# Kernel tuning notes

Measured on AMD Instinct MI355X. Metric: run time of the kernel, lower is better.

Reference implementation:

```python
import jax, jax.numpy as jnp
import numpy as np

SEGMENT_LENGTHS = [1024, 4096]
DILATION_RATES = [1, 2]
HILBERT_CHUNK = 4096
B, N, H, D = 2, 4096, 16, 64


def _hilbert_mapping(n: int) -> np.ndarray:
    """Replicates _generate_hilbert_curve: gather indices for a length-n chunk."""
    if n <= 64:
        return np.arange(n, dtype=np.int64)
    size = 1
    while size * size < n:
        size *= 2

    def d2xy(nn, d):
        x = y = 0
        s = 1
        while s < nn:
            rx = 1 if (d // 2) & 1 else 0
            ry = 1 if (d ^ rx) & 1 else 0
            if ry == 0:
                if rx == 1:
                    x, y = nn - 1 - x, nn - 1 - y
                x, y = y, x
            x += s * rx
            y += s * ry
            d //= 4
            s *= 2
        return x, y

    mapping = np.zeros(n, dtype=np.int64)
    h2l = {}
    for i in range(min(n, size * size)):
        x, y = d2xy(size, i)
        li = y * size + x
        if li < n:
            h2l[i] = li
    hidx = 0
    for i in sorted(h2l):
        mapping[h2l[i]] = hidx
        hidx += 1
    return mapping


def _apply_hilbert(t: jnp.ndarray) -> jnp.ndarray:
    # t: [b, n, h, d]; reorder sequence within HILBERT_CHUNK-sized chunks.
    n = t.shape[1]
    chunks = []
    for start in range(0, n, HILBERT_CHUNK):
        end = min(start + HILBERT_CHUNK, n)
        m = jnp.asarray(_hilbert_mapping(end - start))
        chunks.append(t[:, start:end][:, m])
    return jnp.concatenate(chunks, axis=1) if len(chunks) > 1 else chunks[0]


def _dilation_indices(s: int, r: int, offset: int) -> np.ndarray:
    # Replicates _create_dilation_pattern
    idx = np.arange(offset, s, r, dtype=np.int64)
    expected = (s + r - 1 - offset) // r
    if idx.shape[0] > expected:
        idx = idx[:expected]
    elif idx.shape[0] < expected:
        pad = np.arange(expected - idx.shape[0], dtype=np.int64) % idx.shape[0]
        idx = np.concatenate([idx, idx[pad]])
    return idx


def _dilated_attention(q, k, v):
    # LongNet-style dilated attention: heads partitioned across groups;
    # each group attends within segments over dilated positions.
    b, n, h, d = q.shape
    G = len(SEGMENT_LENGTHS)
    hg = h // G
    scale = 1.0 / np.sqrt(d).astype(np.float32)
    out = jnp.zeros_like(q)
    for g, (s, r) in enumerate(zip(SEGMENT_LENGTHS, DILATION_RATES)):
        offset = g % r
        idx = jnp.asarray(_dilation_indices(s, r, offset))
        hs = slice(g * hg, (g + 1) * hg)
        # [b, n//s, s, hg, d] -> dilated [b, n//s, s/r, hg, d]
        qg = q[:, :, hs].reshape(b, n // s, s, hg, d)[:, :, idx]
        kg = k[:, :, hs].reshape(b, n // s, s, hg, d)[:, :, idx]
        vg = v[:, :, hs].reshape(b, n // s, s, hg, d)[:, :, idx]
        att = jnp.einsum('bgqhd,bgkhd->bghqk', qg, kg) * scale
        att = jax.nn.softmax(att, axis=-1)
        og = jnp.einsum('bghqk,bgkhd->bgqhd', att, vg)
        full = jnp.zeros((b, n // s, s, hg, d), q.dtype).at[:, :, idx].set(og)
        out = out.at[:, :, hs].set(full.reshape(b, n, hg, d))
    return out


def setup_inputs() -> dict:
    key = jax.random.key(0)
    kq, kk, kv = jax.random.split(key, 3)
    q = jax.random.normal(kq, (B, N, H, D), dtype=jnp.float32)
    k = jax.random.normal(kk, (B, N, H, D), dtype=jnp.float32)
    v = jax.random.normal(kv, (B, N, H, D), dtype=jnp.float32)
    return {'q': q, 'k': k, 'v': v}


def reference(q, k, v):
    k_h = _apply_hilbert(k)
    v_h = _apply_hilbert(v)
    return _dilated_attention(q, k_h, v_h)
```

## Files before the change

kernel.cpp:

```cpp
#include <hip/hip_runtime.h>
#include <hip/hip_bf16.h>

#define N_ 4096
#define H_ 16
#define D_ 64
#define G1ROWOFF 65536

typedef __attribute__((ext_vector_type(4))) float f32x4;
typedef __attribute__((ext_vector_type(8))) short bf16x8;

#define AS1 __attribute__((address_space(1)))
#define AS3 __attribute__((address_space(3)))

__device__ __forceinline__ unsigned int cvt2(float a, float b){
  __hip_bfloat16 ha = __float2bfloat16(a);
  __hip_bfloat16 hb = __float2bfloat16(b);
  unsigned short ua, ub;
  __builtin_memcpy(&ua, &ha, 2);
  __builtin_memcpy(&ub, &hb, 2);
  return (unsigned int)ua | ((unsigned int)ub << 16);
}
__device__ __forceinline__ unsigned int pku(unsigned int lo, unsigned int hi){
  return lo | (hi << 16);
}

__global__ __launch_bounds__(1024) void hilbert_map_kernel(int* __restrict__ mapping){
  __shared__ int sm[4096];
  const int t = threadIdx.x;
#pragma unroll
  for(int jj=0;jj<4;jj++) mapping[t*4+jj] = 0;
  int li_a[4], val_a[4];
#pragma unroll
  for(int jj=0;jj<4;jj++){
    int i = t*4+jj;
    int x=0,y=0,d=i;
#pragma unroll
    for(int s=1;s<64;s<<=1){
      int rx=(d>>1)&1;
      int ry=(d^rx)&1;
      if(ry==0){
        if(rx==1){ x=63-x; y=63-y; }
        int tp=x; x=y; y=tp;
      }
      x+=s*rx; y+=s*ry;
      d>>=2;
    }
    int li=y*64+x;
    li_a[jj]=li;
    val_a[jj]=(li<4096)?1:0;
    sm[i]=val_a[jj];
  }
  __syncthreads();
  for(int off=1;off<4096;off<<=1){
    int v[4];
#pragma unroll
    for(int jj=0;jj<4;jj++){
      int i=t*4+jj;
      v[jj]=sm[i]+((i>=off)?sm[i-off]:0);
    }
    __syncthreads();
#pragma unroll
    for(int jj=0;jj<4;jj++) sm[t*4+jj]=v[jj];
    __syncthreads();
  }
#pragma unroll
  for(int jj=0;jj<4;jj++){
    if(val_a[jj]){
      int rank=sm[t*4+jj]-1;
      int li=li_a[jj];
      int wi=(li>=0)?li:(4096+li);
      if(wi>=0 && wi<4096) atomicMax(&mapping[wi], rank);
    }
  }
}

__global__ __launch_bounds__(256) void prep_kv_kernel(
    const float* __restrict__ K, const float* __restrict__ V,
    const int* __restrict__ hmap,
    unsigned short* __restrict__ Kb, unsigned short* __restrict__ Vt)
{
  __shared__ unsigned short Vlds[64*72];
  const int bid = blockIdx.x, tid = threadIdx.x;
  int b, h, dstRowBase, srcRow;
  const int r = tid>>2, part = tid&3;
  if (bid < 1024){
    int t64 = bid&63; h = (bid>>6)&7; b = bid>>9;
    dstRowBase = (b*8+h)*4096 + t64*64;
    srcRow = t64*64 + r;
  } else {
    int bid2 = bid-1024;
    int t64 = bid2&31; int h8 = (bid2>>5)&7; b = bid2>>8; h = 8+h8;
    dstRowBase = G1ROWOFF + (b*8+h8)*2048 + t64*64;
    srcRow = 1 + 2*(t64*64 + r);
  }
  const int src = hmap[srcRow];
  const size_t sb = (((size_t)(b*N_+src))*H_ + h)*D_ + part*16;
  {
    const float4* kp = (const float4*)(K + sb);
    float4 a=kp[0], c=kp[1], e=kp[2], g=kp[3];
    uint4 w0, w1;
    w0.x=cvt2(a.x,a.y); w0.y=cvt2(a.z,a.w); w0.z=cvt2(c.x,c.y); w0.w=cvt2(c.z,c.w);
    w1.x=cvt2(e.x,e.y); w1.y=cvt2(e.z,e.w); w1.z=cvt2(g.x,g.y); w1.w=cvt2(g.z,g.w);
    char* dst = (char*)Kb + ((size_t)(dstRowBase+r))*128;
    *(uint4*)(dst + ((2*part  )^(r&7))*16) = w0;
    *(uint4*)(dst + ((2*part+1)^(r&7))*16) = w1;
  }
  {
    const float4* vp = (const float4*)(V + sb);
    float4 a=vp[0], c=vp[1], e=vp[2], g=vp[3];
    uint4 w0, w1;
    w0.x=cvt2(a.x,a.y); w0.y=cvt2(a.z,a.w); w0.z=cvt2(c.x,c.y); w0.w=cvt2(c.z,c.w);
    w1.x=cvt2(e.x,e.y); w1.y=cvt2(e.z,e.w); w1.z=cvt2(g.x,g.y); w1.w=cvt2(g.z,g.w);
    uint4* dst=(uint4*)&Vlds[r*72 + part*16];
    dst[0]=w0; dst[1]=w1;
  }
  __syncthreads();
  {
    const int d = tid>>2, p2 = tid&3;
    unsigned int w0[4], w1[4];
#pragma unroll
    for(int c=0;c<2;c++){
      int kb = 32*c + 4*p2;
      unsigned int* w = c ? w1 : w0;
      w[0] = pku(Vlds[(kb+ 0)*72+d], Vlds[(kb+ 1)*72+d]);
      w[1] = pku(Vlds[(kb+ 2)*72+d], Vlds[(kb+ 3)*72+d]);
      w[2] = pku(Vlds[(kb+16)*72+d], Vlds[(kb+17)*72+d]);
      w[3] = pku(Vlds[(kb+18)*72+d], Vlds[(kb+19)*72+d]);
    }
    char* dst = (char*)Vt + ((size_t)(dstRowBase+d))*128;
    *(uint4*)(dst + ((p2  )^(d&7))*16) = *(uint4*)w0;
    *(uint4*)(dst + ((p2+4)^(d&7))*16) = *(uint4*)w1;
  }
}

__global__ __launch_bounds__(256, 2) void dilated_attn_kernel(
    const float* __restrict__ Q, const unsigned short* __restrict__ Kb,
    const unsigned short* __restrict__ Vt, float* __restrict__ Out)
{
  __shared__ __align__(16) char smem[65536];

  const int bid = blockIdx.x, tid = threadIdx.x;
  const int wave = tid>>6, lane = tid&63;
  const int lr = lane&15, lg = lane>>4;

  int b, outH, qstep, qoff, njobs, nrj;
  int qloc[2];
  size_t kb0, kb1;
  if (bid < 256){
    int xcd = bid&7, idx = bid>>3;
    int kblk = idx&15, Hp = idx>>4;
    int H = xcd + 8*Hp;
    b = H>>3; outH = 8 + (H&7);
    qstep = 2; qoff = 1; njobs = 1; nrj = 16;
    qloc[0] = kblk*128; qloc[1] = qloc[0];
    size_t rowBase = (size_t)G1ROWOFF + (size_t)H*2048;
    kb0 = rowBase*128; kb1 = kb0 + 16*8192;
    int i = tid>>1, half = tid&1;
    int zpos = 2*(qloc[0] + i);
    float4 z = {0.f,0.f,0.f,0.f};
    float4* op = (float4*)(Out + (((size_t)(b*N_+zpos))*H_ + outH)*D_ + half*32);
#pragma unroll
    for(int j=0;j<8;j++) op[j]=z;
  } else {
    int p = bid - 256;
    int xcd = p&7, idx = p>>3;
    int pair = idx&3, Gp = idx>>2;
    int G = xcd + 8*Gp;
    b = G>>5; int seg=(G>>3)&3; int h=G&7; outH=h;
    qstep = 1; qoff = 0; njobs = 2; nrj = 8;
    qloc[0] = seg*1024 + pair*128;
    qloc[1] = seg*1024 + (pair+4)*128;
    size_t rowBase = ((size_t)(b*8+h))*4096 + (size_t)seg*1024;
    kb0 = rowBase*128; kb1 = kb0;
  }

  const float SCL = 0.125f * 1.4426950408889634f;
  bf16x8 qf[2][2];
  f32x4 acc[2][4];
  f32x4 accl[2];
  const f32x4 FZ = {0.f,0.f,0.f,0.f};
  union{ unsigned int u[4]; bf16x8 v; } ONES;
  ONES.u[0]=0x3F803F80u; ONES.u[1]=0x3F803F80u; ONES.u[2]=0x3F803F80u; ONES.u[3]=0x3F803F80u;

  auto loadQ = [&](int ql0){
#pragma unroll
    for(int qs=0;qs<2;qs++){
      int qpos = qoff + qstep*(ql0 + wave*32 + qs*16 + lr);
      const float* qp = Q + (((size_t)(b*N_+qpos))*H_ + outH)*D_;
#pragma unroll
      for(int dc=0;dc<2;dc++){
        float4 a = *(const float4*)(qp + dc*32 + lg*8);
        float4 c = *(const float4*)(qp + dc*32 + lg*8 + 4);
        union{ unsigned int u[4]; bf16x8 v; } pk;
        pk.u[0]=cvt2(a.x*SCL,a.y*SCL); pk.u[1]=cvt2(a.z*SCL,a.w*SCL);
        pk.u[2]=cvt2(c.x*SCL,c.y*SCL); pk.u[3]=cvt2(c.z*SCL,c.w*SCL);
        qf[qs][dc]=pk.v;
      }
    }
  };

  const int swz = lr&7;
  const int kA0 = lr*128 + ((  lg)^swz)*16;
  const int kA1 = lr*128 + ((4+lg)^swz)*16;
  const int vA0 = 8192 + lr*128 + ((  lg)^swz)*16;
  const int vA1 = 8192 + lr*128 + ((4+lg)^swz)*16;

  const char* gBase = (wave<2) ? (const char*)Kb : (const char*)Vt;
  const int sOff = (tid&127)*16;
  const int sHalf = (wave<2) ? 0 : 8192;
  auto stage = [&](int bufOff, int t){
    size_t off = ((t>=16)? kb1 : kb0) + (size_t)(t&15)*8192 + sOff;
    const char* gsrc = gBase + off;
    char* ldst = smem + bufOff + sHalf + sOff;
#pragma unroll
    for(int i=0;i<4;i++){
      __builtin_amdgcn_global_load_lds((const AS1 void*)(gsrc + i*2048),
                                       (AS3 void*)(ldst + i*2048), 16, 0, 0);
    }
  };

  auto QK = [&](const char* sm, f32x4 (&s)[2][4]){
#pragma unroll
    for(int kt=0;kt<4;kt++){
      bf16x8 k0 = *(const bf16x8*)(sm + kA0 + kt*2048);
      bf16x8 k1 = *(const bf16x8*)(sm + kA1 + kt*2048);
#pragma unroll
      for(int qs=0;qs<2;qs++){
        s[qs][kt] = __builtin_amdgcn_mfma_f32_16x16x32_bf16(k0, qf[qs][0], FZ, 0,0,0);
        s[qs][kt] = __builtin_amdgcn_mfma_f32_16x16x32_bf16(k1, qf[qs][1], s[qs][kt],0,0,0);
      }
    }
  };
  auto SM = [&](const f32x4 (&s)[2][4], bf16x8 (&pf)[2][2]){
#pragma unroll
    for(int qs=0;qs<2;qs++){
      unsigned int U[4][2];
#pragma unroll
      for(int kt=0;kt<4;kt++){
        float p0 = __builtin_amdgcn_exp2f(s[qs][kt][0]);
        float p1 = __builtin_amdgcn_exp2f(s[qs][kt][1]);
        float p2 = __builtin_amdgcn_exp2f(s[qs][kt][2]);
        float p3 = __builtin_amdgcn_exp2f(s[qs][kt][3]);
        U[kt][0] = cvt2(p0,p1);
        U[kt][1] = cvt2(p2,p3);
      }
#pragma unroll
      for(int c=0;c<2;c++){
        union{ unsigned int u[4]; bf16x8 v; } w;
        w.u[0]=U[2*c][0]; w.u[1]=U[2*c][1]; w.u[2]=U[2*c+1][0]; w.u[3]=U[2*c+1][1];
        pf[qs][c] = w.v;
      }
    }
  };
  auto PV = [&](const char* sm, const bf16x8 (&pf)[2][2]){
#pragma unroll
    for(int c=0;c<2;c++){
      const int vAc = c ? vA1 : vA0;
#pragma unroll
      for(int dt=0;dt<4;dt++){
        bf16x8 vf = *(const bf16x8*)(sm + vAc + dt*2048);
        acc[0][dt] = __builtin_amdgcn_mfma_f32_16x16x32_bf16(pf[0][c], vf, acc[0][dt],0,0,0);
        acc[1][dt] = __builtin_amdgcn_mfma_f32_16x16x32_bf16(pf[1][c], vf, acc[1][dt],0,0,0);
      }
      accl[0] = __builtin_amdgcn_mfma_f32_16x16x32_bf16(pf[0][c], ONES.v, accl[0],0,0,0);
      accl[1] = __builtin_amdgcn_mfma_f32_16x16x32_bf16(pf[1][c], ONES.v, accl[1],0,0,0);
    }
  };

  auto epilogue = [&](int ql0){
#pragma unroll
    for(int qs=0;qs<2;qs++)
#pragma unroll
      for(int r=0;r<4;r++){
        float inv = 1.0f/accl[qs][r];
        int qpos = qoff + qstep*(ql0 + wave*32 + qs*16 + lg*4 + r);
        float* op = Out + (((size_t)(b*N_+qpos))*H_ + outH)*D_ + lr;
#pragma unroll
        for(int dt=0;dt<4;dt++) op[dt*16] = acc[qs][dt][r]*inv;
      }
  };

  stage(0, 0); stage(16384, 1);
  int p = 0;
  for(int j=0; j<njobs; ++j){
    loadQ(qloc[j]);
#pragma unroll
    for(int qs=0;qs<2;qs++){
#pragma unroll
      for(int dt=0;dt<4;dt++) acc[qs][dt] = FZ;
      accl[qs] = FZ;
    }
    for(int r=0; r<nrj; ++r, ++p){
      asm volatile("s_waitcnt vmcnt(0)" ::: "memory");
      __builtin_amdgcn_s_barrier();
      const int half = (p&1)*32768;
      if (p < 15){
        const int oth = ((p+1)&1)*32768;
        stage(oth, 2*p+2); stage(oth+16384, 2*p+3);
      }
      const char* smA = smem + half;
      const char* smB = smem + half + 16384;
      f32x4 sA[2][4], sB[2][4];
      bf16x8 pfA[2][2], pfB[2][2];
      QK(smA, sA);
      QK(smB, sB);
      SM(sA, pfA);
      PV(smA, pfA);
      SM(sB, pfB);
      PV(smB, pfB);
    }
    epilogue(qloc[j]);
  }
}

extern "C" void kernel_launch(void* const* d_in, const int* in_sizes, int n_in,
                              void* d_out, int out_size, void* d_ws, size_t ws_size,
                              hipStream_t stream){
  const float* Q = (const float*)d_in[0];
  const float* K = (const float*)d_in[1];
  const float* V = (const float*)d_in[2];
  float* Out = (float*)d_out;

  int* hmap = (int*)d_ws;
  unsigned short* Kb = (unsigned short*)((char*)d_ws + 16384);
  unsigned short* Vt = (unsigned short*)((char*)d_ws + 16384 + 12582912);

  hipLaunchKernelGGL(hilbert_map_kernel, dim3(1), dim3(1024), 0, stream, hmap);
  hipLaunchKernelGGL(prep_kv_kernel, dim3(1536), dim3(256), 0, stream, K, V, hmap, Kb, Vt);
  hipLaunchKernelGGL(dilated_attn_kernel, dim3(512), dim3(256), 0, stream, Q, Kb, Vt, Out);
}
```

Baseline: 71.76 us.

## Switch bf16 to fp16 with pkrtz conversion and interleave softmax with MFMAs

Replaces the bf16 conversions, which take several ALU ops each, with the single packed round-toward-zero fp16 conversion for K, V, Q and the probabilities, and switches the MFMAs to their f16 variants. The inner loop is also hand-scheduled so the exp2 and convert work for one tile is interleaved with the QK MFMAs of the next tile and the PV MFMAs of the current one. The aim is to cut VALU cost and overlap it with matrix work. Risks are fp16 overflow, since softmax runs without max subtraction and exp2 of large scores could exceed the fp16 range, and higher register pressure.

```diff
diff --git a/kernel.cpp b/kernel.cpp
--- a/kernel.cpp
+++ b/kernel.cpp
@@ -7,18 +7,14 @@
 #define G1ROWOFF 65536
 
 typedef __attribute__((ext_vector_type(4))) float f32x4;
-typedef __attribute__((ext_vector_type(8))) short bf16x8;
+typedef __attribute__((ext_vector_type(8))) _Float16 f16x8;
 
 #define AS1 __attribute__((address_space(1)))
 #define AS3 __attribute__((address_space(3)))
 
-__device__ __forceinline__ unsigned int cvt2(float a, float b){
-  __hip_bfloat16 ha = __float2bfloat16(a);
-  __hip_bfloat16 hb = __float2bfloat16(b);
-  unsigned short ua, ub;
-  __builtin_memcpy(&ua, &ha, 2);
-  __builtin_memcpy(&ub, &hb, 2);
-  return (unsigned int)ua | ((unsigned int)ub << 16);
+__device__ __forceinline__ unsigned int pkrtz(float a, float b){
+  auto h = __builtin_amdgcn_cvt_pkrtz(a, b);
+  unsigned int r; __builtin_memcpy(&r, &h, 4); return r;
 }
 __device__ __forceinline__ unsigned int pku(unsigned int lo, unsigned int hi){
   return lo | (hi << 16);
@@ -77,7 +73,7 @@
 __global__ __launch_bounds__(256) void prep_kv_kernel(
     const float* __restrict__ K, const float* __restrict__ V,
     const int* __restrict__ hmap,
-    unsigned short* __restrict__ Kb, unsigned short* __restrict__ Vt)
+    unsigned short* __restrict__ Kh, unsigned short* __restrict__ Vt)
 {
   __shared__ unsigned short Vlds[64*72];
   const int bid = blockIdx.x, tid = threadIdx.x;
@@ -99,9 +95,9 @@
     const float4* kp = (const float4*)(K + sb);
     float4 a=kp[0], c=kp[1], e=kp[2], g=kp[3];
     uint4 w0, w1;
-    w0.x=cvt2(a.x,a.y); w0.y=cvt2(a.z,a.w); w0.z=cvt2(c.x,c.y); w0.w=cvt2(c.z,c.w);
-    w1.x=cvt2(e.x,e.y); w1.y=cvt2(e.z,e.w); w1.z=cvt2(g.x,g.y); w1.w=cvt2(g.z,g.w);
-    char* dst = (char*)Kb + ((size_t)(dstRowBase+r))*128;
+    w0.x=pkrtz(a.x,a.y); w0.y=pkrtz(a.z,a.w); w0.z=pkrtz(c.x,c.y); w0.w=pkrtz(c.z,c.w);
+    w1.x=pkrtz(e.x,e.y); w1.y=pkrtz(e.z,e.w); w1.z=pkrtz(g.x,g.y); w1.w=pkrtz(g.z,g.w);
+    char* dst = (char*)Kh + ((size_t)(dstRowBase+r))*128;
     *(uint4*)(dst + ((2*part  )^(r&7))*16) = w0;
     *(uint4*)(dst + ((2*part+1)^(r&7))*16) = w1;
   }
@@ -109,8 +105,8 @@
     const float4* vp = (const float4*)(V + sb);
     float4 a=vp[0], c=vp[1], e=vp[2], g=vp[3];
     uint4 w0, w1;
-    w0.x=cvt2(a.x,a.y); w0.y=cvt2(a.z,a.w); w0.z=cvt2(c.x,c.y); w0.w=cvt2(c.z,c.w);
-    w1.x=cvt2(e.x,e.y); w1.y=cvt2(e.z,e.w); w1.z=cvt2(g.x,g.y); w1.w=cvt2(g.z,g.w);
+    w0.x=pkrtz(a.x,a.y); w0.y=pkrtz(a.z,a.w); w0.z=pkrtz(c.x,c.y); w0.w=pkrtz(c.z,c.w);
+    w1.x=pkrtz(e.x,e.y); w1.y=pkrtz(e.z,e.w); w1.z=pkrtz(g.x,g.y); w1.w=pkrtz(g.z,g.w);
     uint4* dst=(uint4*)&Vlds[r*72 + part*16];
     dst[0]=w0; dst[1]=w1;
   }
@@ -134,7 +130,7 @@
 }
 
 __global__ __launch_bounds__(256, 2) void dilated_attn_kernel(
-    const float* __restrict__ Q, const unsigned short* __restrict__ Kb,
+    const float* __restrict__ Q, const unsigned short* __restrict__ Kh,
     const unsigned short* __restrict__ Vt, float* __restrict__ Out)
 {
   __shared__ __align__(16) char smem[65536];
@@ -175,12 +171,12 @@
   }
 
   const float SCL = 0.125f * 1.4426950408889634f;
-  bf16x8 qf[2][2];
+  f16x8 qf[2][2];
   f32x4 acc[2][4];
   f32x4 accl[2];
   const f32x4 FZ = {0.f,0.f,0.f,0.f};
-  union{ unsigned int u[4]; bf16x8 v; } ONES;
-  ONES.u[0]=0x3F803F80u; ONES.u[1]=0x3F803F80u; ONES.u[2]=0x3F803F80u; ONES.u[3]=0x3F803F80u;
+  union{ unsigned int u[4]; f16x8 v; } ONES;
+  ONES.u[0]=0x3C003C00u; ONES.u[1]=0x3C003C00u; ONES.u[2]=0x3C003C00u; ONES.u[3]=0x3C003C00u;
 
   auto loadQ = [&](int ql0){
 #pragma unroll
@@ -191,9 +187,9 @@
       for(int dc=0;dc<2;dc++){
         float4 a = *(const float4*)(qp + dc*32 + lg*8);
         float4 c = *(const float4*)(qp + dc*32 + lg*8 + 4);
-        union{ unsigned int u[4]; bf16x8 v; } pk;
-        pk.u[0]=cvt2(a.x*SCL,a.y*SCL); pk.u[1]=cvt2(a.z*SCL,a.w*SCL);
-        pk.u[2]=cvt2(c.x*SCL,c.y*SCL); pk.u[3]=cvt2(c.z*SCL,c.w*SCL);
+        union{ unsigned int u[4]; f16x8 v; } pk;
+        pk.u[0]=pkrtz(a.x*SCL,a.y*SCL); pk.u[1]=pkrtz(a.z*SCL,a.w*SCL);
+        pk.u[2]=pkrtz(c.x*SCL,c.y*SCL); pk.u[3]=pkrtz(c.z*SCL,c.w*SCL);
         qf[qs][dc]=pk.v;
       }
     }
@@ -205,7 +201,7 @@
   const int vA0 = 8192 + lr*128 + ((  lg)^swz)*16;
   const int vA1 = 8192 + lr*128 + ((4+lg)^swz)*16;
 
-  const char* gBase = (wave<2) ? (const char*)Kb : (const char*)Vt;
+  const char* gBase = (wave<2) ? (const char*)Kh : (const char*)Vt;
   const int sOff = (tid&127)*16;
   const int sHalf = (wave<2) ? 0 : 8192;
   auto stage = [&](int bufOff, int t){
@@ -216,54 +212,6 @@
     for(int i=0;i<4;i++){
       __builtin_amdgcn_global_load_lds((const AS1 void*)(gsrc + i*2048),
                                        (AS3 void*)(ldst + i*2048), 16, 0, 0);
-    }
-  };
-
-  auto QK = [&](const char* sm, f32x4 (&s)[2][4]){
-#pragma unroll
-    for(int kt=0;kt<4;kt++){
-      bf16x8 k0 = *(const bf16x8*)(sm + kA0 + kt*2048);
-      bf16x8 k1 = *(const bf16x8*)(sm + kA1 + kt*2048);
-#pragma unroll
-      for(int qs=0;qs<2;qs++){
-        s[qs][kt] = __builtin_amdgcn_mfma_f32_16x16x32_bf16(k0, qf[qs][0], FZ, 0,0,0);
-        s[qs][kt] = __builtin_amdgcn_mfma_f32_16x16x32_bf16(k1, qf[qs][1], s[qs][kt],0,0,0);
-      }
-    }
-  };
-  auto SM = [&](const f32x4 (&s)[2][4], bf16x8 (&pf)[2][2]){
-#pragma unroll
-    for(int qs=0;qs<2;qs++){
-      unsigned int U[4][2];
-#pragma unroll
-      for(int kt=0;kt<4;kt++){
-        float p0 = __builtin_amdgcn_exp2f(s[qs][kt][0]);
-        float p1 = __builtin_amdgcn_exp2f(s[qs][kt][1]);
-        float p2 = __builtin_amdgcn_exp2f(s[qs][kt][2]);
-        float p3 = __builtin_amdgcn_exp2f(s[qs][kt][3]);
-        U[kt][0] = cvt2(p0,p1);
-        U[kt][1] = cvt2(p2,p3);
-      }
-#pragma unroll
-      for(int c=0;c<2;c++){
-        union{ unsigned int u[4]; bf16x8 v; } w;
-        w.u[0]=U[2*c][0]; w.u[1]=U[2*c][1]; w.u[2]=U[2*c+1][0]; w.u[3]=U[2*c+1][1];
-        pf[qs][c] = w.v;
-      }
-    }
-  };
-  auto PV = [&](const char* sm, const bf16x8 (&pf)[2][2]){
-#pragma unroll
-    for(int c=0;c<2;c++){
-      const int vAc = c ? vA1 : vA0;
-#pragma unroll
-      for(int dt=0;dt<4;dt++){
-        bf16x8 vf = *(const bf16x8*)(sm + vAc + dt*2048);
-        acc[0][dt] = __builtin_amdgcn_mfma_f32_16x16x32_bf16(pf[0][c], vf, acc[0][dt],0,0,0);
-        acc[1][dt] = __builtin_amdgcn_mfma_f32_16x16x32_bf16(pf[1][c], vf, acc[1][dt],0,0,0);
-      }
-      accl[0] = __builtin_amdgcn_mfma_f32_16x16x32_bf16(pf[0][c], ONES.v, accl[0],0,0,0);
-      accl[1] = __builtin_amdgcn_mfma_f32_16x16x32_bf16(pf[1][c], ONES.v, accl[1],0,0,0);
     }
   };
 
@@ -300,14 +248,79 @@
       }
       const char* smA = smem + half;
       const char* smB = smem + half + 16384;
+
       f32x4 sA[2][4], sB[2][4];
-      bf16x8 pfA[2][2], pfB[2][2];
-      QK(smA, sA);
-      QK(smB, sB);
-      SM(sA, pfA);
-      PV(smA, pfA);
-      SM(sB, pfB);
-      PV(smB, pfB);
+#pragma unroll
+      for(int kt=0;kt<4;kt++){
+        f16x8 k0 = *(const f16x8*)(smA + kA0 + kt*2048);
+        f16x8 k1 = *(const f16x8*)(smA + kA1 + kt*2048);
+#pragma unroll
+        for(int qs=0;qs<2;qs++){
+          sA[qs][kt] = __builtin_amdgcn_mfma_f32_16x16x32_f16(k0, qf[qs][0], FZ, 0,0,0);
+          sA[qs][kt] = __builtin_amdgcn_mfma_f32_16x16x32_f16(k1, qf[qs][1], sA[qs][kt],0,0,0);
+        }
+      }
+
+      unsigned int UA[2][4][2], UB[2][4][2];
+#pragma unroll
+      for(int kt=0;kt<4;kt++){
+        f16x8 k0 = *(const f16x8*)(smB + kA0 + kt*2048);
+        f16x8 k1 = *(const f16x8*)(smB + kA1 + kt*2048);
+        sB[0][kt] = __builtin_amdgcn_mfma_f32_16x16x32_f16(k0, qf[0][0], FZ, 0,0,0);
+        UA[0][kt][0] = pkrtz(__builtin_amdgcn_exp2f(sA[0][kt][0]),
+                             __builtin_amdgcn_exp2f(sA[0][kt][1]));
+        sB[0][kt] = __builtin_amdgcn_mfma_f32_16x16x32_f16(k1, qf[0][1], sB[0][kt],0,0,0);
+        UA[0][kt][1] = pkrtz(__builtin_amdgcn_exp2f(sA[0][kt][2]),
+                             __builtin_amdgcn_exp2f(sA[0][kt][3]));
+        sB[1][kt] = __builtin_amdgcn_mfma_f32_16x16x32_f16(k0, qf[1][0], FZ, 0,0,0);
+        UA[1][kt][0] = pkrtz(__builtin_amdgcn_exp2f(sA[1][kt][0]),
+                             __builtin_amdgcn_exp2f(sA[1][kt][1]));
+        sB[1][kt] = __builtin_amdgcn_mfma_f32_16x16x32_f16(k1, qf[1][1], sB[1][kt],0,0,0);
+        UA[1][kt][1] = pkrtz(__builtin_amdgcn_exp2f(sA[1][kt][2]),
+                             __builtin_amdgcn_exp2f(sA[1][kt][3]));
+      }
+      union{ unsigned int u[4]; f16x8 v; } pfA[2][2];
+#pragma unroll
+      for(int qs=0;qs<2;qs++)
+#pragma unroll
+        for(int c=0;c<2;c++){
+          pfA[qs][c].u[0]=UA[qs][2*c][0]; pfA[qs][c].u[1]=UA[qs][2*c][1];
+          pfA[qs][c].u[2]=UA[qs][2*c+1][0]; pfA[qs][c].u[3]=UA[qs][2*c+1][1];
+        }
+
+#pragma unroll
+      for(int c=0;c<2;c++){
+        const int vAc = c ? vA1 : vA0;
+#pragma unroll
+        for(int dt=0;dt<4;dt++){
+          f16x8 vf = *(const f16x8*)(smA + vAc + dt*2048);
+          const int bqs = dt>>1, bkt = 2*c + (dt&1);
+          acc[0][dt] = __builtin_amdgcn_mfma_f32_16x16x32_f16(pfA[0][c].v, vf, acc[0][dt],0,0,0);
+          UB[bqs][bkt][0] = pkrtz(__builtin_amdgcn_exp2f(sB[bqs][bkt][0]),
+                                  __builtin_amdgcn_exp2f(sB[bqs][bkt][1]));
+          acc[1][dt] = __builtin_amdgcn_mfma_f32_16x16x32_f16(pfA[1][c].v, vf, acc[1][dt],0,0,0);
+          UB[bqs][bkt][1] = pkrtz(__builtin_amdgcn_exp2f(sB[bqs][bkt][2]),
+                                  __builtin_amdgcn_exp2f(sB[bqs][bkt][3]));
+        }
+        accl[0] = __builtin_amdgcn_mfma_f32_16x16x32_f16(pfA[0][c].v, ONES.v, accl[0],0,0,0);
+        accl[1] = __builtin_amdgcn_mfma_f32_16x16x32_f16(pfA[1][c].v, ONES.v, accl[1],0,0,0);
+      }
+
+#pragma unroll
+      for(int c=0;c<2;c++){
+        union{ unsigned int u[4]; f16x8 v; } pf0, pf1;
+        pf0.u[0]=UB[0][2*c][0]; pf0.u[1]=UB[0][2*c][1]; pf0.u[2]=UB[0][2*c+1][0]; pf0.u[3]=UB[0][2*c+1][1];
+        pf1.u[0]=UB[1][2*c][0]; pf1.u[1]=UB[1][2*c][1]; pf1.u[2]=UB[1][2*c+1][0]; pf1.u[3]=UB[1][2*c+1][1];
+        const int vAc = c ? vA1 : vA0;
+#pragma unroll
+        for(int dt=0;dt<4;dt++){
+          f16x8 vf = *(const f16x8*)(smB + vAc + dt*2048);
+          acc[0][dt] = __builtin_amdgcn_mfma_f32_16x16x32_f16(pf0.v, vf, acc[0][dt],0,0,0);
+          acc[1][dt] = __builtin_amdgcn_mfma_f32_16x16x32_f16(pf1.v, vf, acc[1][dt],0,0,0);
+        }
+        accl[0] = __builtin_amdgcn_mfma_f32_16x16x32_f16(pf0.v, ONES.v, accl[0],0,0,0);
+        accl[1] = __builtin_amdgcn_mfma_f32_16x16x32_f16(pf1.v, ONES.v, accl[1],0,0,0);
+      }
     }
     epilogue(qloc[j]);
   }
@@ -322,10 +335,10 @@
   float* Out = (float*)d_out;
 
   int* hmap = (int*)d_ws;
-  unsigned short* Kb = (unsigned short*)((char*)d_ws + 16384);
+  unsigned short* Kh = (unsigned short*)((char*)d_ws + 16384);
   unsigned short* Vt = (unsigned short*)((char*)d_ws + 16384 + 12582912);
 
   hipLaunchKernelGGL(hilbert_map_kernel, dim3(1), dim3(1024), 0, stream, hmap);
-  hipLaunchKernelGGL(prep_kv_kernel, dim3(1536), dim3(256), 0, stream, K, V, hmap, Kb, Vt);
-  hipLaunchKernelGGL(dilated_attn_kernel, dim3(512), dim3(256), 0, stream, Q, Kb, Vt, Out);
-}
+  hipLaunchKernelGGL(prep_kv_kernel, dim3(1536), dim3(256), 0, stream, K, V, hmap, Kh, Vt);
+  hipLaunchKernelGGL(dilated_attn_kernel, dim3(512), dim3(256), 0, stream, Q, Kh, Vt, Out);
+}
```

Result: faster. 67.70 us (-5.7%).
